# Optimization experiments

Hardware: AMD Instinct MI355X
Metric: run time of the kernel (lower is better)

The kernel has to match this reference:

```python
import jax, jax.numpy as jnp
import numpy as np

B, C, H, W = 4, 2048, 32, 32


def conv1x1(x, Wt, b):
    # 1x1 conv == per-pixel matmul over channels
    return jnp.einsum('oc,bchw->bohw', Wt, x) + b[None, :, None, None]


def cross_attention(Q, K, V):
    b, c, h, w = Q.shape
    q = Q.reshape(b, c, h * w)   # [B, C, N]
    k = K.reshape(b, c, h * w)
    v = V.reshape(b, c, h * w)
    scores = jnp.einsum('bcn,bcm->bnm', q, k) / jnp.sqrt(jnp.asarray(c, jnp.float32))
    attn = jax.nn.softmax(scores, axis=-1)          # [B, N, N]
    out = jnp.einsum('bcm,bnm->bcn', v, attn)       # V @ attn^T
    return out.reshape(b, c, h, w)


def setup_inputs() -> dict:
    key = jax.random.key(0)
    ks = jax.random.split(key, 14)
    d = {
        'F_rgb': jax.random.normal(ks[0], (B, C, H, W), jnp.float32),
        'F_indices': jax.random.normal(ks[1], (B, C, H, W), jnp.float32),
    }
    names = ['q_rgb', 'k_rgb', 'v_rgb', 'q_ind', 'k_ind', 'v_ind']
    for i, n in enumerate(names):
        d['W_' + n] = jax.random.normal(ks[2 + 2 * i], (C, C), jnp.float32) * 0.02
        d['b_' + n] = jax.random.normal(ks[3 + 2 * i], (C,), jnp.float32) * 0.01
    return d


def reference(F_rgb, F_indices, W_q_rgb, b_q_rgb, W_k_rgb, b_k_rgb, W_v_rgb, b_v_rgb,
              W_q_ind, b_q_ind, W_k_ind, b_k_ind, W_v_ind, b_v_ind):
    # RGB queries attend over index features
    Q_rgb = conv1x1(F_rgb, W_q_rgb, b_q_rgb)
    K_ind = conv1x1(F_indices, W_k_ind, b_k_ind)
    V_ind = conv1x1(F_indices, W_v_ind, b_v_ind)
    F_rgb_attended = cross_attention(Q_rgb, K_ind, V_ind)
    # Index queries attend over RGB features
    Q_ind = conv1x1(F_indices, W_q_ind, b_q_ind)
    K_rgb = conv1x1(F_rgb, W_k_rgb, b_k_rgb)
    V_rgb = conv1x1(F_rgb, W_v_rgb, b_v_rgb)
    F_ind_attended = cross_attention(Q_ind, K_rgb, V_rgb)
    F_final = F_rgb_attended + F_ind_attended
    attention_weights = jnp.stack([F_rgb_attended, F_ind_attended], axis=1)  # [B,2,C,H,W]
    # pre_attention_outputs is an identity passthrough of the inputs
    return (F_final, F_rgb, F_indices, attention_weights)
```

## Files before the change

### kernel.cpp

```cpp
#include <hip/hip_runtime.h>

typedef __bf16 bf16x8 __attribute__((ext_vector_type(8)));
typedef float  f32x4  __attribute__((ext_vector_type(4)));
typedef unsigned short u16;
typedef unsigned short u16x8 __attribute__((ext_vector_type(8)));

__device__ __forceinline__ u16 f2bf(float f) {
  unsigned u = __builtin_bit_cast(unsigned, f);
  u += 0x7fffu + ((u >> 16) & 1u);
  return (u16)(u >> 16);
}
__device__ __forceinline__ float bf2f(u16 h) {
  return __builtin_bit_cast(float, (unsigned)h << 16);
}

using gvoid = __attribute__((address_space(1))) void;
using svoid = __attribute__((address_space(3))) void;
__device__ __forceinline__ void load_lds16(const void* g, void* s) {
  __builtin_amdgcn_global_load_lds((const gvoid*)g, (svoid*)s, 16, 0, 0);
}

__global__ void prep(const float* __restrict__ Fr, const float* __restrict__ Fi,
                     u16* __restrict__ FTr, u16* __restrict__ FTi,
                     float* __restrict__ Or, float* __restrict__ Oi,
                     const float* __restrict__ s0, const float* __restrict__ s1,
                     const float* __restrict__ s2, const float* __restrict__ s3,
                     const float* __restrict__ s4, const float* __restrict__ s5,
                     u16* __restrict__ Wall) {
  const int tx = threadIdx.x, ty = threadIdx.y;
  const int t2 = ty * 32 + tx;
  if (blockIdx.z >= 8) {
    const int gi = (blockIdx.z - 8) * 1024 + blockIdx.y * 32 + blockIdx.x;
    const int chunk = gi >> 12;
    const int i = (gi & 4095) * 256 + t2;
    const float* src;
    switch (chunk) {
      case 0: src = s0; break; case 1: src = s1; break; case 2: src = s2; break;
      case 3: src = s3; break; case 4: src = s4; break; default: src = s5; break;
    }
    float4 v = ((const float4*)src)[i];
    ushort4 o;
    o.x = f2bf(v.x); o.y = f2bf(v.y); o.z = f2bf(v.z); o.w = f2bf(v.w);
    ((ushort4*)(Wall + (long)chunk * 4194304))[i] = o;
    return;
  }
  __shared__ float tile[64][33];
  const int b = blockIdx.z & 3;
  const bool ind = (blockIdx.z >= 4);
  const float* F = ind ? Fi : Fr;
  u16* FT = ind ? FTi : FTr;
  float* O = ind ? Oi : Or;
  const int n0 = blockIdx.x * 32, c0 = blockIdx.y * 64;
  const long boff = (long)b * 2048 * 1024;
  const float* Fb = F + boff;
  float* Ob = O + boff;
  u16* FTb = FT + (long)b * 1024 * 2048;
#pragma unroll
  for (int i = 0; i < 8; ++i) {
    const long idx = (long)(c0 + ty + i * 8) * 1024 + n0 + tx;
    float v = Fb[idx];
    tile[ty + i * 8][tx] = v;
    Ob[idx] = v;
  }
  __syncthreads();
  const int q = t2 & 7, r = t2 >> 3;
  u16x8 o8;
#pragma unroll
  for (int k = 0; k < 8; ++k) o8[k] = f2bf(tile[8 * q + k][r]);
  *(u16x8*)(FTb + (long)(n0 + r) * 2048 + c0 + 8 * q) = o8;
}

#define BAR_ do { asm volatile("" ::: "memory"); __builtin_amdgcn_s_barrier(); \
                  asm volatile("" ::: "memory"); } while (0)
#define SB0 __builtin_amdgcn_sched_barrier(0)
#define LGK0 asm volatile("s_waitcnt lgkmcnt(0)" ::: "memory")
#define VMW6 asm volatile("s_waitcnt vmcnt(6)" ::: "memory")
#define VMW0 asm volatile("s_waitcnt vmcnt(0)" ::: "memory")

#define b0A0 0
#define b0A1 16384
#define b0B0 32768
#define b0B1 49152
#define b1A0 65536
#define b1A1 81920
#define b1B0 98304
#define b1B1 114688

#define STG(Mp, ld, row0, kt, off)                                                 \
  do {                                                                             \
    load_lds16(Mp + (long)((row0) + w * 8 + srow) * (ld) + (kt) * 64 + scol,       \
               sm + (off) + w * 1024);                                             \
    load_lds16(Mp + (long)((row0) + 64 + w * 8 + srow) * (ld) + (kt) * 64 + scol,  \
               sm + (off) + 8192 + w * 1024);                                      \
  } while (0)

#define RDA(off)                                                                   \
  _Pragma("unroll") for (int fm = 0; fm < 4; ++fm)                                 \
  _Pragma("unroll") for (int ks = 0; ks < 2; ++ks)                                 \
    fa[fm][ks] = *(const bf16x8*)(sm + (off) + aoff[fm] + kin[ks]);

#define RDB(off, dst)                                                              \
  _Pragma("unroll") for (int fn = 0; fn < 2; ++fn)                                 \
  _Pragma("unroll") for (int ks = 0; ks < 2; ++ks)                                 \
    dst[fn][ks] = *(const bf16x8*)(sm + (off) + boff[fn] + kin[ks]);

#define MMQ2(qa)                                                                   \
  __builtin_amdgcn_s_setprio(1);                                                   \
  _Pragma("unroll") for (int ks = 0; ks < 2; ++ks)                                 \
  _Pragma("unroll") for (int fm = 0; fm < 4; ++fm) {                               \
    _Pragma("unroll") for (int fn = 0; fn < 2; ++fn)                               \
      acc[qa][0][fm][fn] = __builtin_amdgcn_mfma_f32_16x16x32_bf16(                \
          fa[fm][ks], fb0[fn][ks], acc[qa][0][fm][fn], 0, 0, 0);                   \
    _Pragma("unroll") for (int fn = 0; fn < 2; ++fn)                               \
      acc[qa][1][fm][fn] = __builtin_amdgcn_mfma_f32_16x16x32_bf16(                \
          fa[fm][ks], fb1[fn][ks], acc[qa][1][fm][fn], 0, 0, 0);                   \
  }                                                                                \
  __builtin_amdgcn_s_setprio(0);

#define GEMM_LOOP                                                                  \
  STG(Ag, lda, m0,       0, b0A0);                                                 \
  STG(Bg, ldb, n0,       0, b0B0);                                                 \
  STG(Bg, ldb, n0 + 128, 0, b0B1);                                                 \
  STG(Ag, lda, m0 + 128, 0, b0A1);                                                 \
  STG(Ag, lda, m0,       1, b1A0);                                                 \
  STG(Bg, ldb, n0,       1, b1B0);                                                 \
  STG(Bg, ldb, n0 + 128, 1, b1B1);                                                 \
  VMW6;                                                                            \
  BAR_;                                                                            \
  for (int v = 0; v < nt; v += 2) {                                                \
    const int t2 = (v + 2 < nt) ? v + 2 : nt - 1;                                  \
    const int t3 = (v + 3 < nt) ? v + 3 : nt - 1;                                  \
    STG(Ag, lda, m0 + 128, v + 1, b1A1);                                           \
    RDA(b0A0); RDB(b0B0, fb0); RDB(b0B1, fb1);                                     \
    BAR_; LGK0; SB0; MMQ2(0);                                                      \
    STG(Ag, lda, m0, t2, b0A0);                                                    \
    STG(Bg, ldb, n0, t2, b0B0);                                                    \
    STG(Bg, ldb, n0 + 128, t2, b0B1);                                              \
    RDA(b0A1);                                                                     \
    VMW6;                                                                          \
    BAR_; LGK0; SB0; MMQ2(1);                                                      \
    STG(Ag, lda, m0 + 128, t2, b0A1);                                              \
    RDA(b1A0); RDB(b1B0, fb0); RDB(b1B1, fb1);                                     \
    BAR_; LGK0; SB0; MMQ2(0);                                                      \
    STG(Ag, lda, m0, t3, b1A0);                                                    \
    STG(Bg, ldb, n0, t3, b1B0);                                                    \
    STG(Bg, ldb, n0 + 128, t3, b1B1);                                              \
    RDA(b1A1);                                                                     \
    VMW6;                                                                          \
    BAR_; LGK0; SB0; MMQ2(1);                                                      \
  }

#define GEMM_LOCALS                                                                \
  const int t = threadIdx.x, w = t >> 6, l = t & 63;                               \
  const int wr = w >> 2, wc = w & 3;                                               \
  const int lm = l & 15, lk = l >> 4;                                              \
  const int swz = (l & 7) << 4;                                                    \
  const int srow = l >> 3;                                                         \
  const int scol = ((l & 7) ^ srow) << 3;                                          \
  int aoff[4], boff[2], kin[2];                                                    \
  _Pragma("unroll") for (int fm = 0; fm < 4; ++fm)                                 \
    aoff[fm] = (wr * 64 + fm * 16 + lm) * 128;                                     \
  _Pragma("unroll") for (int fn = 0; fn < 2; ++fn)                                 \
    boff[fn] = (wc * 32 + fn * 16 + lm) * 128;                                     \
  kin[0] = (lk * 16) ^ swz;                                                        \
  kin[1] = (64 + lk * 16) ^ swz;                                                   \
  f32x4 acc[2][2][4][2] = {};                                                      \
  bf16x8 fa[4][2], fb0[2][2], fb1[2][2];

template <int OUT_BF16, int BIAS_MODE, int KSPLIT>
__global__ __launch_bounds__(512, 2) void gemm256(
    const u16* __restrict__ A0p, const u16* __restrict__ B0p, void* __restrict__ D0p,
    const float* __restrict__ ba0, const float* __restrict__ bb0,
    const u16* __restrict__ A1p, const u16* __restrict__ B1p, void* __restrict__ D1p,
    const float* __restrict__ ba1, const float* __restrict__ bb1,
    long sKH, int zsplit, int K, int lda, int ldb, int ldd,
    long sA, long sB, long sD) {
  __shared__ __attribute__((aligned(128))) char sm[131072];
  const int gx = gridDim.x, gy = gridDim.y;
  const int nwg = gx * gy * (int)gridDim.z;
  const int lin = blockIdx.x + gx * (blockIdx.y + gy * blockIdx.z);
  const int qch = nwg >> 3;
  int swzid = (lin & 7) * qch + (lin >> 3);
  const int bx = swzid % gx; swzid /= gx;
  const int by = swzid % gy;
  int zb = swzid / gy;
  int kh = 0;
  if (KSPLIT) { kh = zb >> 3; zb &= 7; }
  const bool s1 = (zb >= zsplit);
  const int zz = s1 ? zb - zsplit : zb;
  const u16* Ag = (s1 ? A1p : A0p) + (long)zz * sA + (long)kh * K;
  const u16* Bg = (s1 ? B1p : B0p) + (long)zz * sB + (long)kh * K;
  char* Dg = (char*)(s1 ? D1p : D0p) + (long)zz * sD * (OUT_BF16 ? 2 : 4)
           + (KSPLIT ? (long)kh * sKH : 0L);
  const float* ba = s1 ? ba1 : ba0;
  const float* bb = s1 ? bb1 : bb0;
  const int m0 = by * 256, n0 = bx * 256;
  GEMM_LOCALS
  const int nt = K >> 6;

  GEMM_LOOP

  VMW0;
  const int esz = OUT_BF16 ? 2 : 4;
#pragma unroll
  for (int qa = 0; qa < 2; ++qa)
#pragma unroll
    for (int fm = 0; fm < 4; ++fm) {
      BAR_;
#pragma unroll
      for (int qb = 0; qb < 2; ++qb)
#pragma unroll
        for (int fn = 0; fn < 2; ++fn) {
          const int col = qb * 128 + wc * 32 + fn * 16 + lm;
          const f32x4 vv = acc[qa][qb][fm][fn];
#pragma unroll
          for (int j = 0; j < 4; ++j) {
            const int r = wr * 16 + lk * 4 + j;
            float x = vv[j];
            if (BIAS_MODE == 1) {
              const int gc = n0 + col;
              x += (gc < 2048) ? ba[gc] : bb[gc - 2048];
            }
            if (BIAS_MODE == 2)
              x += ba[m0 + qa * 128 + wr * 64 + fm * 16 + lk * 4 + j];
            if (OUT_BF16) ((u16*)sm)[r * 256 + col] = f2bf(x);
            else          ((float*)sm)[r * 256 + col] = x;
          }
        }
      LGK0;
      BAR_;
#pragma unroll
      for (int p = 0; p < (OUT_BF16 ? 2 : 4); ++p) {
        const int off = p * 8192 + t * 16;
        const int r = OUT_BF16 ? (off >> 9) : (off >> 10);
        const int inrow = OUT_BF16 ? (off & 511) : (off & 1023);
        const int grow = m0 + qa * 128 + (r >> 4) * 64 + fm * 16 + (r & 15);
        const f32x4 d = *(const f32x4*)(sm + off);
        *(f32x4*)(Dg + ((long)grow * ldd + n0) * esz + inrow) = d;
      }
    }
}

__global__ __launch_bounds__(512, 2) void gemm_qkv(
    const u16* __restrict__ FT_r, const u16* __restrict__ FT_i,
    const u16* __restrict__ Wqk_r, const u16* __restrict__ Wqk_i,
    const u16* __restrict__ Wv_r, const u16* __restrict__ Wv_i,
    u16* __restrict__ QKT_r, u16* __restrict__ QKT_i,
    u16* __restrict__ V_r, u16* __restrict__ V_i,
    const float* __restrict__ bq_r, const float* __restrict__ bk_r,
    const float* __restrict__ bq_i, const float* __restrict__ bk_i,
    const float* __restrict__ bv_r, const float* __restrict__ bv_i) {
  __shared__ __attribute__((aligned(128))) char sm[131072];
  const int lin = blockIdx.x;
  const int id = (lin & 7) * 96 + (lin >> 3);
  const u16* Ag; const u16* Bg; u16* Dg;
  const float* ba; const float* bb;
  int lda, ldb, ldd, m0, n0, biasmode;
  if (id < 512) {
    const int bx = id & 15, by = (id >> 4) & 3, zb = id >> 6;
    const bool ind = (zb >= 4);
    const int zz = zb & 3;
    Ag = (ind ? FT_i : FT_r) + (long)zz * 2097152L;
    Bg = ind ? Wqk_i : Wqk_r;
    Dg = (ind ? QKT_i : QKT_r) + (long)zz * 4194304L;
    ba = ind ? bq_i : bq_r;
    bb = ind ? bk_i : bk_r;
    lda = 2048; ldb = 2048; ldd = 4096;
    m0 = by * 256; n0 = bx * 256; biasmode = 1;
  } else {
    const int id2 = id - 512;
    const int bx = id2 & 3, by = (id2 >> 2) & 7, zb = id2 >> 5;
    const bool ind = (zb >= 4);
    const int zz = zb & 3;
    Ag = ind ? Wv_i : Wv_r;
    Bg = (ind ? FT_i : FT_r) + (long)zz * 2097152L;
    Dg = (ind ? V_i : V_r) + (long)zz * 2097152L;
    ba = ind ? bv_i : bv_r;
    bb = nullptr;
    lda = 2048; ldb = 2048; ldd = 1024;
    m0 = by * 256; n0 = bx * 256; biasmode = 2;
  }
  GEMM_LOCALS
  const int nt = 32;

  GEMM_LOOP

  VMW0;
#pragma unroll
  for (int qa = 0; qa < 2; ++qa)
#pragma unroll
    for (int fm = 0; fm < 4; ++fm) {
      BAR_;
#pragma unroll
      for (int qb = 0; qb < 2; ++qb)
#pragma unroll
        for (int fn = 0; fn < 2; ++fn) {
          const int col = qb * 128 + wc * 32 + fn * 16 + lm;
          const f32x4 vv = acc[qa][qb][fm][fn];
#pragma unroll
          for (int j = 0; j < 4; ++j) {
            const int r = wr * 16 + lk * 4 + j;
            float x = vv[j];
            if (biasmode == 1) {
              const int gc = n0 + col;
              x += (gc < 2048) ? ba[gc] : bb[gc - 2048];
            } else {
              x += ba[m0 + qa * 128 + wr * 64 + fm * 16 + lk * 4 + j];
            }
            ((u16*)sm)[r * 256 + col] = f2bf(x);
          }
        }
      LGK0;
      BAR_;
#pragma unroll
      for (int p = 0; p < 2; ++p) {
        const int off = p * 8192 + t * 16;
        const int r = off >> 9;
        const int inrow = off & 511;
        const int grow = m0 + qa * 128 + (r >> 4) * 64 + fm * 16 + (r & 15);
        const f32x4 d = *(const f32x4*)(sm + off);
        *(f32x4*)((char*)Dg + ((long)grow * ldd + n0) * 2 + inrow) = d;
      }
    }
}

__global__ void softmax_rows2(const u16* __restrict__ S0, const u16* __restrict__ S1,
                              u16* __restrict__ P, float alpha) {
  const long row = blockIdx.x;
  const int t = threadIdx.x, l = t & 63, w = t >> 6;
  ushort4 a = ((const ushort4*)(S0 + row * 1024))[t];
  ushort4 b = ((const ushort4*)(S1 + row * 1024))[t];
  float v0 = bf2f(a.x) + bf2f(b.x);
  float v1 = bf2f(a.y) + bf2f(b.y);
  float v2 = bf2f(a.z) + bf2f(b.z);
  float v3 = bf2f(a.w) + bf2f(b.w);
  __shared__ float red[8];
  float m = fmaxf(fmaxf(v0, v1), fmaxf(v2, v3));
#pragma unroll
  for (int off = 32; off; off >>= 1) m = fmaxf(m, __shfl_xor(m, off));
  if (l == 0) red[w] = m;
  __syncthreads();
  m = fmaxf(fmaxf(red[0], red[1]), fmaxf(red[2], red[3]));
  float e0 = __expf((v0 - m) * alpha);
  float e1 = __expf((v1 - m) * alpha);
  float e2 = __expf((v2 - m) * alpha);
  float e3 = __expf((v3 - m) * alpha);
  float s = e0 + e1 + e2 + e3;
#pragma unroll
  for (int off = 32; off; off >>= 1) s += __shfl_xor(s, off);
  if (l == 0) red[4 + w] = s;
  __syncthreads();
  s = red[4] + red[5] + red[6] + red[7];
  const float inv = 1.0f / s;
  ushort4 o;
  o.x = f2bf(e0 * inv); o.y = f2bf(e1 * inv);
  o.z = f2bf(e2 * inv); o.w = f2bf(e3 * inv);
  ((ushort4*)(P + row * 1024))[t] = o;
}

__global__ void final_add(const float4* __restrict__ aw, float4* __restrict__ dst) {
  const long i = (long)blockIdx.x * 256 + threadIdx.x;
  const long b = i >> 19;
  const long r = i & 524287;
  float4 a = aw[b * 1048576 + r];
  float4 c = aw[b * 1048576 + 524288 + r];
  float4 o;
  o.x = a.x + c.x; o.y = a.y + c.y; o.z = a.z + c.z; o.w = a.w + c.w;
  dst[i] = o;
}

extern "C" void kernel_launch(void* const* d_in, const int* in_sizes, int n_in,
                              void* d_out, int out_size, void* d_ws, size_t ws_size,
                              hipStream_t stream) {
  (void)in_sizes; (void)n_in; (void)out_size; (void)ws_size;
  const float* F_rgb = (const float*)d_in[0];
  const float* F_ind = (const float*)d_in[1];
  const float* bq_rgb = (const float*)d_in[3];
  const float* bk_rgb = (const float*)d_in[5];
  const float* bv_rgb = (const float*)d_in[7];
  const float* bq_ind = (const float*)d_in[9];
  const float* bk_ind = (const float*)d_in[11];
  const float* bv_ind = (const float*)d_in[13];

  char* ws = (char*)d_ws;
  u16* FT_rgb  = (u16*)(ws);
  u16* FT_ind  = (u16*)(ws + 16777216);
  u16* S1c     = (u16*)(ws);
  u16* Wall    = (u16*)(ws + 33554432);
  u16* Wqk_rgb = Wall;
  u16* Wqk_ind = (u16*)(ws + 50331648);
  u16* Wv_rgb  = (u16*)(ws + 67108864);
  u16* Wv_ind  = (u16*)(ws + 75497472);
  u16* QKT_rgb = (u16*)(ws + 83886080);
  u16* QKT_ind = (u16*)(ws + 117440512);
  u16* V_rgb   = (u16*)(ws + 150994944);
  u16* V_ind   = (u16*)(ws + 167772160);
  u16* S0c     = (u16*)(ws + 184549376);
  u16* P       = (u16*)(ws + 218103808);

  float* out       = (float*)d_out;
  float* out_final = out;
  float* out_Frgb  = out + 8388608;
  float* out_Find  = out + 16777216;
  float* AW        = out + 25165824;

  prep<<<dim3(32, 32, 32), dim3(32, 8), 0, stream>>>(
      F_rgb, F_ind, FT_rgb, FT_ind, out_Frgb, out_Find,
      (const float*)d_in[2], (const float*)d_in[4],
      (const float*)d_in[8], (const float*)d_in[10],
      (const float*)d_in[6], (const float*)d_in[12], Wall);

  gemm_qkv<<<768, 512, 0, stream>>>(
      FT_rgb, FT_ind, Wqk_rgb, Wqk_ind, Wv_rgb, Wv_ind,
      QKT_rgb, QKT_ind, V_rgb, V_ind,
      bq_rgb, bk_rgb, bq_ind, bk_ind, bv_rgb, bv_ind);

  gemm256<1, 0, 1><<<dim3(4, 4, 16), 512, 0, stream>>>(
      QKT_rgb, QKT_ind + 2048, S0c, nullptr, nullptr,
      QKT_ind, QKT_rgb + 2048, S0c + 4194304, nullptr, nullptr,
      (long)((char*)S1c - (char*)S0c), 4, 1024, 4096, 4096, 1024,
      4194304L, 4194304L, 1048576L);

  softmax_rows2<<<8192, 256, 0, stream>>>(S0c, S1c, P, 0.02209708691207961f);

  gemm256<0, 0, 0><<<dim3(4, 8, 8), 512, 0, stream>>>(
      V_ind, P, AW, nullptr, nullptr,
      V_rgb, P + 4194304, AW + 2097152, nullptr, nullptr,
      0L, 4, 1024, 1024, 1024, 1024, 2097152L, 1048576L, 4194304L);

  final_add<<<8192, 256, 0, stream>>>((const float4*)AW, (float4*)out_final);
}
```

Before: 321.3 us.

## Co-schedule V projection with non-split score GEMM and drop split-K sum

Q/K projections now run alone in the templated 256-tile GEMM. The V projection and the QK^T score GEMM share one 384-block kernel, with the score GEMM now covering the full K range instead of splitting K in two. Softmax then reads a single score buffer instead of summing two partial buffers. The aim is to cut wave-quantization tails (768 blocks before, now 512 plus 384) and the extra partial-score traffic. The cost is that each score block runs twice as many K iterations, so load balance inside the combined kernel may suffer.

```diff
diff --git a/kernel.cpp b/kernel.cpp
--- a/kernel.cpp
+++ b/kernel.cpp
@@ -241,44 +241,39 @@
     }
 }
 
-__global__ __launch_bounds__(512, 2) void gemm_qkv(
+__global__ __launch_bounds__(512, 2) void gemm_vs(
     const u16* __restrict__ FT_r, const u16* __restrict__ FT_i,
-    const u16* __restrict__ Wqk_r, const u16* __restrict__ Wqk_i,
     const u16* __restrict__ Wv_r, const u16* __restrict__ Wv_i,
-    u16* __restrict__ QKT_r, u16* __restrict__ QKT_i,
     u16* __restrict__ V_r, u16* __restrict__ V_i,
-    const float* __restrict__ bq_r, const float* __restrict__ bk_r,
-    const float* __restrict__ bq_i, const float* __restrict__ bk_i,
+    const u16* __restrict__ QKT_r, const u16* __restrict__ QKT_i,
+    u16* __restrict__ S,
     const float* __restrict__ bv_r, const float* __restrict__ bv_i) {
   __shared__ __attribute__((aligned(128))) char sm[131072];
   const int lin = blockIdx.x;
-  const int id = (lin & 7) * 96 + (lin >> 3);
-  const u16* Ag; const u16* Bg; u16* Dg;
-  const float* ba; const float* bb;
-  int lda, ldb, ldd, m0, n0, biasmode;
-  if (id < 512) {
-    const int bx = id & 15, by = (id >> 4) & 3, zb = id >> 6;
-    const bool ind = (zb >= 4);
-    const int zz = zb & 3;
-    Ag = (ind ? FT_i : FT_r) + (long)zz * 2097152L;
-    Bg = ind ? Wqk_i : Wqk_r;
-    Dg = (ind ? QKT_i : QKT_r) + (long)zz * 4194304L;
-    ba = ind ? bq_i : bq_r;
-    bb = ind ? bk_i : bk_r;
-    lda = 2048; ldb = 2048; ldd = 4096;
-    m0 = by * 256; n0 = bx * 256; biasmode = 1;
-  } else {
-    const int id2 = id - 512;
-    const int bx = id2 & 3, by = (id2 >> 2) & 7, zb = id2 >> 5;
+  const int id = (lin & 7) * 48 + (lin >> 3);
+  const u16* Ag; const u16* Bg; u16* Dg; const float* ba;
+  int lda, ldb, ldd, m0, n0;
+  if (id < 256) {
+    const int bx = id & 3, by = (id >> 2) & 7, zb = id >> 5;
     const bool ind = (zb >= 4);
     const int zz = zb & 3;
     Ag = ind ? Wv_i : Wv_r;
     Bg = (ind ? FT_i : FT_r) + (long)zz * 2097152L;
     Dg = (ind ? V_i : V_r) + (long)zz * 2097152L;
     ba = ind ? bv_i : bv_r;
-    bb = nullptr;
     lda = 2048; ldb = 2048; ldd = 1024;
-    m0 = by * 256; n0 = bx * 256; biasmode = 2;
+    m0 = by * 256; n0 = bx * 256;
+  } else {
+    const int id2 = id - 256;
+    const int bx = id2 & 3, by = (id2 >> 2) & 3, zb = id2 >> 4;
+    const bool d1 = (zb >= 4);
+    const int zz = zb & 3;
+    Ag = (d1 ? QKT_i : QKT_r) + (long)zz * 4194304L;
+    Bg = (d1 ? QKT_r : QKT_i) + 2048 + (long)zz * 4194304L;
+    Dg = S + (d1 ? 4194304L : 0L) + (long)zz * 1048576L;
+    ba = nullptr;
+    lda = 4096; ldb = 4096; ldd = 1024;
+    m0 = by * 256; n0 = bx * 256;
   }
   GEMM_LOCALS
   const int nt = 32;
@@ -301,12 +296,7 @@
           for (int j = 0; j < 4; ++j) {
             const int r = wr * 16 + lk * 4 + j;
             float x = vv[j];
-            if (biasmode == 1) {
-              const int gc = n0 + col;
-              x += (gc < 2048) ? ba[gc] : bb[gc - 2048];
-            } else {
-              x += ba[m0 + qa * 128 + wr * 64 + fm * 16 + lk * 4 + j];
-            }
+            if (ba) x += ba[m0 + qa * 128 + wr * 64 + fm * 16 + lk * 4 + j];
             ((u16*)sm)[r * 256 + col] = f2bf(x);
           }
         }
@@ -324,16 +314,12 @@
     }
 }
 
-__global__ void softmax_rows2(const u16* __restrict__ S0, const u16* __restrict__ S1,
-                              u16* __restrict__ P, float alpha) {
+__global__ void softmax_rows1(const u16* __restrict__ S, u16* __restrict__ P,
+                              float alpha) {
   const long row = blockIdx.x;
   const int t = threadIdx.x, l = t & 63, w = t >> 6;
-  ushort4 a = ((const ushort4*)(S0 + row * 1024))[t];
-  ushort4 b = ((const ushort4*)(S1 + row * 1024))[t];
-  float v0 = bf2f(a.x) + bf2f(b.x);
-  float v1 = bf2f(a.y) + bf2f(b.y);
-  float v2 = bf2f(a.z) + bf2f(b.z);
-  float v3 = bf2f(a.w) + bf2f(b.w);
+  ushort4 a = ((const ushort4*)(S + row * 1024))[t];
+  float v0 = bf2f(a.x), v1 = bf2f(a.y), v2 = bf2f(a.z), v3 = bf2f(a.w);
   __shared__ float red[8];
   float m = fmaxf(fmaxf(v0, v1), fmaxf(v2, v3));
 #pragma unroll
@@ -385,7 +371,6 @@
   char* ws = (char*)d_ws;
   u16* FT_rgb  = (u16*)(ws);
   u16* FT_ind  = (u16*)(ws + 16777216);
-  u16* S1c     = (u16*)(ws);
   u16* Wall    = (u16*)(ws + 33554432);
   u16* Wqk_rgb = Wall;
   u16* Wqk_ind = (u16*)(ws + 50331648);
@@ -395,7 +380,7 @@
   u16* QKT_ind = (u16*)(ws + 117440512);
   u16* V_rgb   = (u16*)(ws + 150994944);
   u16* V_ind   = (u16*)(ws + 167772160);
-  u16* S0c     = (u16*)(ws + 184549376);
+  u16* S       = (u16*)(ws + 184549376);
   u16* P       = (u16*)(ws + 218103808);
 
   float* out       = (float*)d_out;
@@ -410,18 +395,16 @@
       (const float*)d_in[8], (const float*)d_in[10],
       (const float*)d_in[6], (const float*)d_in[12], Wall);
 
-  gemm_qkv<<<768, 512, 0, stream>>>(
-      FT_rgb, FT_ind, Wqk_rgb, Wqk_ind, Wv_rgb, Wv_ind,
-      QKT_rgb, QKT_ind, V_rgb, V_ind,
-      bq_rgb, bk_rgb, bq_ind, bk_ind, bv_rgb, bv_ind);
-
-  gemm256<1, 0, 1><<<dim3(4, 4, 16), 512, 0, stream>>>(
-      QKT_rgb, QKT_ind + 2048, S0c, nullptr, nullptr,
-      QKT_ind, QKT_rgb + 2048, S0c + 4194304, nullptr, nullptr,
-      (long)((char*)S1c - (char*)S0c), 4, 1024, 4096, 4096, 1024,
-      4194304L, 4194304L, 1048576L);
-
-  softmax_rows2<<<8192, 256, 0, stream>>>(S0c, S1c, P, 0.02209708691207961f);
+  gemm256<1, 1, 0><<<dim3(16, 4, 8), 512, 0, stream>>>(
+      FT_rgb, Wqk_rgb, QKT_rgb, bq_rgb, bk_rgb,
+      FT_ind, Wqk_ind, QKT_ind, bq_ind, bk_ind,
+      0L, 4, 2048, 2048, 2048, 4096, 2097152L, 0L, 4194304L);
+
+  gemm_vs<<<384, 512, 0, stream>>>(
+      FT_rgb, FT_ind, Wv_rgb, Wv_ind, V_rgb, V_ind,
+      QKT_rgb, QKT_ind, S, bv_rgb, bv_ind);
+
+  softmax_rows1<<<8192, 256, 0, stream>>>(S, P, 0.02209708691207961f);
 
   gemm256<0, 0, 0><<<dim3(4, 8, 8), 512, 0, stream>>>(
       V_ind, P, AW, nullptr, nullptr,
```

Measured after the change: 345.5 us. +7.5%, slower.
